# Optimization experiments

Measured on AMD Instinct MI355X. Metric: run time of the kernel, lower is better.

The kernel has to match this reference:

```python
import jax, jax.numpy as jnp
import numpy as np

TEMPERATURE = 0.5


def setup_inputs() -> dict:
    key = jax.random.key(0)
    k1, k2 = jax.random.split(key)
    N, D = 8192, 128
    features = jax.random.normal(k1, (N, D), dtype=jnp.float32)
    labels = jax.random.randint(k2, (N,), 0, 10, dtype=jnp.int64)
    return {"features": features, "labels": labels}


def reference(features, labels):
    # cosine similarity via normalized matmul (fused form of the broadcasted version)
    eps = 1e-8
    norm = jnp.maximum(jnp.linalg.norm(features, axis=-1, keepdims=True), eps)
    fn = features / norm
    sim = jnp.einsum('id,jd->ij', fn, fn) / TEMPERATURE  # [N, N]

    pos_mask = labels[:, None] == labels[None, :]        # [N, N] bool
    pos_f = pos_mask.astype(sim.dtype)
    neg_f = 1.0 - pos_f

    exp_pos = jnp.exp(sim * pos_f)                       # [N, N]
    exp_neg = jnp.sum(jnp.exp(sim * neg_f), axis=1, keepdims=True)  # [N, 1]

    loss_mat = -jnp.log(exp_pos / (exp_pos + exp_neg))   # [N, N]
    # mean over positive entries (jit-safe masked mean)
    num_pos = jnp.sum(pos_f)
    loss = jnp.sum(loss_mat * pos_f) / num_pos
    return loss
```

## Files before the change

### kernel.cpp

```cpp
#include <hip/hip_runtime.h>
#include <hip/hip_bf16.h>
#include <math.h>

#define NROWS 8192
#define DIM 128
#define BM 128
#define BN 128
#define CS 8
#define COLS_PER_SLAB (NROWS / CS)
#define CT_ITERS (COLS_PER_SLAB / BN)
#define RS (NROWS / BM)

typedef __attribute__((ext_vector_type(8))) short bf16x8;
typedef __attribute__((ext_vector_type(4))) float f32x4;

__global__ __launch_bounds__(1024) void k_hist(const int* __restrict__ lab,
                                               int* __restrict__ hist,
                                               float* __restrict__ losssum) {
  __shared__ int sh[16][16];
  const int t = threadIdx.x;
  const int w = t >> 6;
  if ((t & 63) < 16) sh[w][t & 63] = 0;
  __syncthreads();
#pragma unroll
  for (int it = 0; it < NROWS / 1024; ++it)
    atomicAdd(&sh[w][lab[t + it * 1024]], 1);
  __syncthreads();
  if (t < 10) {
    int s = 0;
#pragma unroll
    for (int x = 0; x < 16; ++x) s += sh[x][t];
    hist[t] = s;
  }
  if (t == 10) losssum[0] = 0.f;
}

__global__ __launch_bounds__(256) void k_norm(const float* __restrict__ f,
                                              __hip_bfloat16* __restrict__ fnb) {
  int wave = threadIdx.x >> 6;
  int lane = threadIdx.x & 63;
  int row = blockIdx.x * 4 + wave;
  const float* src = f + (size_t)row * DIM;
  float v0 = src[lane];
  float v1 = src[lane + 64];
  float ss = v0 * v0 + v1 * v1;
#pragma unroll
  for (int o = 32; o > 0; o >>= 1) ss += __shfl_down(ss, o);
  ss = __shfl(ss, 0);
  float inv = 1.0f / fmaxf(sqrtf(ss), 1e-8f);
  __hip_bfloat16* dst = fnb + (size_t)row * DIM;
  dst[lane] = __float2bfloat16(v0 * inv);
  dst[lane + 64] = __float2bfloat16(v1 * inv);
}

__global__ __launch_bounds__(256, 2) void k_main(
    const ushort* __restrict__ fnb, const int* __restrict__ lab,
    float* __restrict__ pneg, float* __restrict__ ppos,
    float* __restrict__ ppos2, float* __restrict__ psim) {
  __shared__ char lds[BM * 256 + BN * 256];
  char* Alds = lds;
  char* Blds = lds + BM * 256;

  const int t = threadIdx.x;
  const int lane = t & 63;
  const int w = t >> 6;
  const int wm = w >> 1;
  const int wn = w & 1;
  const int cs = blockIdx.x;
  const int i0 = blockIdx.y * BM;

  {
    const int4* src = reinterpret_cast<const int4*>(fnb + (size_t)i0 * DIM);
#pragma unroll
    for (int it = 0; it < 8; ++it) {
      int q = t + 256 * it;
      int row = q >> 4, c = q & 15;
      int4 v = src[q];
      *reinterpret_cast<int4*>(Alds + row * 256 + ((c << 4) ^ ((row & 7) << 4))) = v;
    }
  }

  int lr[4][4];
#pragma unroll
  for (int m = 0; m < 4; ++m)
#pragma unroll
    for (int r = 0; r < 4; ++r)
      lr[m][r] = lab[i0 + wm * 64 + m * 16 + (lane >> 4) * 4 + r];

  float a_neg[4][4] = {}, a_pos[4][4] = {}, a_pos2[4][4] = {}, a_sim[4][4] = {};

  for (int ct = 0; ct < CT_ITERS; ++ct) {
    const int j0 = cs * COLS_PER_SLAB + ct * BN;
    __syncthreads();
    {
      const int4* src = reinterpret_cast<const int4*>(fnb + (size_t)j0 * DIM);
#pragma unroll
      for (int it = 0; it < 8; ++it) {
        int q = t + 256 * it;
        int row = q >> 4, c = q & 15;
        int4 v = src[q];
        *reinterpret_cast<int4*>(Blds + row * 256 + ((c << 4) ^ ((row & 7) << 4))) = v;
      }
    }
    __syncthreads();

    f32x4 acc[4][4];
#pragma unroll
    for (int m = 0; m < 4; ++m)
#pragma unroll
      for (int n = 0; n < 4; ++n) acc[m][n] = (f32x4){0.f, 0.f, 0.f, 0.f};

#pragma unroll
    for (int ks = 0; ks < 4; ++ks) {
      const int kb = ks * 64 + ((lane >> 4) << 4);
      bf16x8 af[4], bf[4];
#pragma unroll
      for (int m = 0; m < 4; ++m) {
        int r = wm * 64 + m * 16 + (lane & 15);
        af[m] = *reinterpret_cast<const bf16x8*>(Alds + r * 256 + (kb ^ ((r & 7) << 4)));
      }
#pragma unroll
      for (int n = 0; n < 4; ++n) {
        int r = wn * 64 + n * 16 + (lane & 15);
        bf[n] = *reinterpret_cast<const bf16x8*>(Blds + r * 256 + (kb ^ ((r & 7) << 4)));
      }
#pragma unroll
      for (int m = 0; m < 4; ++m)
#pragma unroll
        for (int n = 0; n < 4; ++n)
          acc[m][n] = __builtin_amdgcn_mfma_f32_16x16x32_bf16(af[m], bf[n], acc[m][n], 0, 0, 0);
    }

#pragma unroll
    for (int n = 0; n < 4; ++n) {
      const int lc = lab[j0 + wn * 64 + n * 16 + (lane & 15)];
#pragma unroll
      for (int m = 0; m < 4; ++m)
#pragma unroll
        for (int r = 0; r < 4; ++r) {
          float s = acc[m][n][r];
          float E = __expf(2.0f * s);
          bool pos = (lr[m][r] == lc);
          a_neg[m][r] += pos ? 0.f : E;
          a_pos[m][r] += pos ? E : 0.f;
          a_pos2[m][r] += pos ? E * E : 0.f;
          a_sim[m][r] += pos ? s : 0.f;
        }
    }
  }

#pragma unroll
  for (int m = 0; m < 4; ++m)
#pragma unroll
    for (int r = 0; r < 4; ++r)
#pragma unroll
      for (int off = 8; off > 0; off >>= 1) {
        a_neg[m][r] += __shfl_xor(a_neg[m][r], off);
        a_pos[m][r] += __shfl_xor(a_pos[m][r], off);
        a_pos2[m][r] += __shfl_xor(a_pos2[m][r], off);
        a_sim[m][r] += __shfl_xor(a_sim[m][r], off);
      }

  __syncthreads();
  float* red = reinterpret_cast<float*>(lds);
  const int g = lane >> 4;
  if (wn == 1 && (lane & 15) == 0) {
#pragma unroll
    for (int m = 0; m < 4; ++m)
#pragma unroll
      for (int r = 0; r < 4; ++r) {
        int rl = wm * 64 + m * 16 + g * 4 + r;
        red[rl * 4 + 0] = a_neg[m][r];
        red[rl * 4 + 1] = a_pos[m][r];
        red[rl * 4 + 2] = a_pos2[m][r];
        red[rl * 4 + 3] = a_sim[m][r];
      }
  }
  __syncthreads();
  if (wn == 0 && (lane & 15) == 0) {
#pragma unroll
    for (int m = 0; m < 4; ++m)
#pragma unroll
      for (int r = 0; r < 4; ++r) {
        int rl = wm * 64 + m * 16 + g * 4 + r;
        int row = i0 + rl;
        pneg[cs * NROWS + row] = a_neg[m][r] + red[rl * 4 + 0];
        ppos[cs * NROWS + row] = a_pos[m][r] + red[rl * 4 + 1];
        ppos2[cs * NROWS + row] = a_pos2[m][r] + red[rl * 4 + 2];
        psim[cs * NROWS + row] = a_sim[m][r] + red[rl * 4 + 3];
      }
  }
}

__global__ __launch_bounds__(1024) void k_rowfinal(
    const float* __restrict__ pneg, const float* __restrict__ ppos,
    const float* __restrict__ ppos2, const float* __restrict__ psim,
    const int* __restrict__ lab, const int* __restrict__ hist,
    float* __restrict__ losssum) {
  __shared__ float sred[1024];
  int i = blockIdx.x * 1024 + threadIdx.x;
  float ns = 0.f, ps = 0.f, ps2 = 0.f, sa = 0.f;
#pragma unroll
  for (int cs = 0; cs < CS; ++cs) {
    ns += pneg[cs * NROWS + i];
    ps += ppos[cs * NROWS + i];
    ps2 += ppos2[cs * NROWS + i];
    sa += psim[cs * NROWS + i];
  }
  float cnt = (float)hist[lab[i]];
  float negtot = ns + cnt;
  float li = cnt * logf(negtot) - 2.f * sa + ps / negtot - ps2 / (2.f * negtot * negtot);
  sred[threadIdx.x] = li;
  __syncthreads();
  for (int s2 = 512; s2 > 0; s2 >>= 1) {
    if (threadIdx.x < s2) sred[threadIdx.x] += sred[threadIdx.x + s2];
    __syncthreads();
  }
  if (threadIdx.x == 0) atomicAdd(losssum, sred[0]);
}

__global__ void k_out(const float* __restrict__ losssum, const int* __restrict__ hist,
                      float* __restrict__ out) {
  if (threadIdx.x == 0) {
    double np = 0.0;
    for (int c = 0; c < 10; ++c) np += (double)hist[c] * (double)hist[c];
    out[0] = (float)((double)losssum[0] / np);
  }
}

extern "C" void kernel_launch(void* const* d_in, const int* in_sizes, int n_in,
                              void* d_out, int out_size, void* d_ws, size_t ws_size,
                              hipStream_t stream) {
  const float* feat = (const float*)d_in[0];
  const int* lab = (const int*)d_in[1];
  float* out = (float*)d_out;

  char* ws = (char*)d_ws;
  __hip_bfloat16* fnb = (__hip_bfloat16*)ws;
  size_t off = (size_t)NROWS * DIM * 2;
  float* pneg = (float*)(ws + off);  off += (size_t)CS * NROWS * 4;
  float* ppos = (float*)(ws + off);  off += (size_t)CS * NROWS * 4;
  float* ppos2 = (float*)(ws + off); off += (size_t)CS * NROWS * 4;
  float* psim = (float*)(ws + off);  off += (size_t)CS * NROWS * 4;
  int* hist = (int*)(ws + off);      off += 64;
  float* losssum = (float*)(ws + off);

  k_hist<<<1, 1024, 0, stream>>>(lab, hist, losssum);
  k_norm<<<NROWS / 4, 256, 0, stream>>>(feat, fnb);
  dim3 grid(CS, RS);
  k_main<<<grid, 256, 0, stream>>>((const ushort*)fnb, lab, pneg, ppos, ppos2, psim);
  k_rowfinal<<<NROWS / 1024, 1024, 0, stream>>>(pneg, ppos, ppos2, psim, lab, hist, losssum);
  k_out<<<1, 64, 0, stream>>>(losssum, hist, out);
}
```

Baseline: 60.53 us.

## Fold temperature scale into normalization and drop squared-positive accumulator

Features are pre-scaled by sqrt(2) during normalization, so the GEMM output is already sim/T and the exp needs no extra multiply. The main kernel now accumulates the total exp sum and derives the negative sum as total minus positive, and it drops the E^2 positive accumulator and its second-order correction term. The histogram kernel is folded into the row-final kernel, which removes one launch, and the cross-wave reduction is simplified. This cuts per-element epilogue ALU work, shuffles and partial-buffer traffic, but it changes the approximation of log(1+x) by dropping a correction term, which may shift accuracy.

```diff
diff --git a/kernel.cpp b/kernel.cpp
--- a/kernel.cpp
+++ b/kernel.cpp
@@ -10,33 +10,15 @@
 #define COLS_PER_SLAB (NROWS / CS)
 #define CT_ITERS (COLS_PER_SLAB / BN)
 #define RS (NROWS / BM)
+#define SQRT2 1.41421356237309515f
 
 typedef __attribute__((ext_vector_type(8))) short bf16x8;
 typedef __attribute__((ext_vector_type(4))) float f32x4;
 
-__global__ __launch_bounds__(1024) void k_hist(const int* __restrict__ lab,
-                                               int* __restrict__ hist,
-                                               float* __restrict__ losssum) {
-  __shared__ int sh[16][16];
-  const int t = threadIdx.x;
-  const int w = t >> 6;
-  if ((t & 63) < 16) sh[w][t & 63] = 0;
-  __syncthreads();
-#pragma unroll
-  for (int it = 0; it < NROWS / 1024; ++it)
-    atomicAdd(&sh[w][lab[t + it * 1024]], 1);
-  __syncthreads();
-  if (t < 10) {
-    int s = 0;
-#pragma unroll
-    for (int x = 0; x < 16; ++x) s += sh[x][t];
-    hist[t] = s;
-  }
-  if (t == 10) losssum[0] = 0.f;
-}
-
 __global__ __launch_bounds__(256) void k_norm(const float* __restrict__ f,
-                                              __hip_bfloat16* __restrict__ fnb) {
+                                              __hip_bfloat16* __restrict__ fnb,
+                                              float* __restrict__ losssum) {
+  if (blockIdx.x == 0 && threadIdx.x == 0) losssum[0] = 0.f;
   int wave = threadIdx.x >> 6;
   int lane = threadIdx.x & 63;
   int row = blockIdx.x * 4 + wave;
@@ -47,7 +29,7 @@
 #pragma unroll
   for (int o = 32; o > 0; o >>= 1) ss += __shfl_down(ss, o);
   ss = __shfl(ss, 0);
-  float inv = 1.0f / fmaxf(sqrtf(ss), 1e-8f);
+  float inv = SQRT2 / fmaxf(sqrtf(ss), 1e-8f);
   __hip_bfloat16* dst = fnb + (size_t)row * DIM;
   dst[lane] = __float2bfloat16(v0 * inv);
   dst[lane + 64] = __float2bfloat16(v1 * inv);
@@ -55,8 +37,7 @@
 
 __global__ __launch_bounds__(256, 2) void k_main(
     const ushort* __restrict__ fnb, const int* __restrict__ lab,
-    float* __restrict__ pneg, float* __restrict__ ppos,
-    float* __restrict__ ppos2, float* __restrict__ psim) {
+    float* __restrict__ ptot, float* __restrict__ ppos, float* __restrict__ psim) {
   __shared__ char lds[BM * 256 + BN * 256];
   char* Alds = lds;
   char* Blds = lds + BM * 256;
@@ -66,6 +47,8 @@
   const int w = t >> 6;
   const int wm = w >> 1;
   const int wn = w & 1;
+  const int g = lane >> 4;
+  const int li16 = lane & 15;
   const int cs = blockIdx.x;
   const int i0 = blockIdx.y * BM;
 
@@ -85,9 +68,9 @@
   for (int m = 0; m < 4; ++m)
 #pragma unroll
     for (int r = 0; r < 4; ++r)
-      lr[m][r] = lab[i0 + wm * 64 + m * 16 + (lane >> 4) * 4 + r];
-
-  float a_neg[4][4] = {}, a_pos[4][4] = {}, a_pos2[4][4] = {}, a_sim[4][4] = {};
+      lr[m][r] = lab[i0 + wm * 64 + m * 16 + g * 4 + r];
+
+  float a_tot[4][4] = {}, a_pos[4][4] = {}, a_sim[4][4] = {};
 
   for (int ct = 0; ct < CT_ITERS; ++ct) {
     const int j0 = cs * COLS_PER_SLAB + ct * BN;
@@ -112,16 +95,16 @@
 
 #pragma unroll
     for (int ks = 0; ks < 4; ++ks) {
-      const int kb = ks * 64 + ((lane >> 4) << 4);
+      const int kb = ks * 64 + (g << 4);
       bf16x8 af[4], bf[4];
 #pragma unroll
       for (int m = 0; m < 4; ++m) {
-        int r = wm * 64 + m * 16 + (lane & 15);
+        int r = wm * 64 + m * 16 + li16;
         af[m] = *reinterpret_cast<const bf16x8*>(Alds + r * 256 + (kb ^ ((r & 7) << 4)));
       }
 #pragma unroll
       for (int n = 0; n < 4; ++n) {
-        int r = wn * 64 + n * 16 + (lane & 15);
+        int r = wn * 64 + n * 16 + li16;
         bf[n] = *reinterpret_cast<const bf16x8*>(Blds + r * 256 + (kb ^ ((r & 7) << 4)));
       }
 #pragma unroll
@@ -133,17 +116,16 @@
 
 #pragma unroll
     for (int n = 0; n < 4; ++n) {
-      const int lc = lab[j0 + wn * 64 + n * 16 + (lane & 15)];
+      const int lc = lab[j0 + wn * 64 + n * 16 + li16];
 #pragma unroll
       for (int m = 0; m < 4; ++m)
 #pragma unroll
         for (int r = 0; r < 4; ++r) {
           float s = acc[m][n][r];
-          float E = __expf(2.0f * s);
+          float E = __expf(s);
           bool pos = (lr[m][r] == lc);
-          a_neg[m][r] += pos ? 0.f : E;
+          a_tot[m][r] += E;
           a_pos[m][r] += pos ? E : 0.f;
-          a_pos2[m][r] += pos ? E * E : 0.f;
           a_sim[m][r] += pos ? s : 0.f;
         }
     }
@@ -155,77 +137,92 @@
     for (int r = 0; r < 4; ++r)
 #pragma unroll
       for (int off = 8; off > 0; off >>= 1) {
-        a_neg[m][r] += __shfl_xor(a_neg[m][r], off);
+        a_tot[m][r] += __shfl_xor(a_tot[m][r], off);
         a_pos[m][r] += __shfl_xor(a_pos[m][r], off);
-        a_pos2[m][r] += __shfl_xor(a_pos2[m][r], off);
         a_sim[m][r] += __shfl_xor(a_sim[m][r], off);
       }
 
   __syncthreads();
-  float* red = reinterpret_cast<float*>(lds);
-  const int g = lane >> 4;
-  if (wn == 1 && (lane & 15) == 0) {
+  float(*red)[2][3] = reinterpret_cast<float(*)[2][3]>(lds);
+  if (li16 == 0) {
 #pragma unroll
     for (int m = 0; m < 4; ++m)
 #pragma unroll
       for (int r = 0; r < 4; ++r) {
         int rl = wm * 64 + m * 16 + g * 4 + r;
-        red[rl * 4 + 0] = a_neg[m][r];
-        red[rl * 4 + 1] = a_pos[m][r];
-        red[rl * 4 + 2] = a_pos2[m][r];
-        red[rl * 4 + 3] = a_sim[m][r];
-      }
-  }
-  __syncthreads();
-  if (wn == 0 && (lane & 15) == 0) {
+        red[rl][wn][0] = a_tot[m][r];
+        red[rl][wn][1] = a_pos[m][r];
+        red[rl][wn][2] = a_sim[m][r];
+      }
+  }
+  __syncthreads();
+  if (wn == 0 && li16 == 0) {
 #pragma unroll
     for (int m = 0; m < 4; ++m)
 #pragma unroll
       for (int r = 0; r < 4; ++r) {
         int rl = wm * 64 + m * 16 + g * 4 + r;
         int row = i0 + rl;
-        pneg[cs * NROWS + row] = a_neg[m][r] + red[rl * 4 + 0];
-        ppos[cs * NROWS + row] = a_pos[m][r] + red[rl * 4 + 1];
-        ppos2[cs * NROWS + row] = a_pos2[m][r] + red[rl * 4 + 2];
-        psim[cs * NROWS + row] = a_sim[m][r] + red[rl * 4 + 3];
+        ptot[(size_t)cs * NROWS + row] = red[rl][0][0] + red[rl][1][0];
+        ppos[(size_t)cs * NROWS + row] = red[rl][0][1] + red[rl][1][1];
+        psim[(size_t)cs * NROWS + row] = red[rl][0][2] + red[rl][1][2];
       }
   }
 }
 
 __global__ __launch_bounds__(1024) void k_rowfinal(
-    const float* __restrict__ pneg, const float* __restrict__ ppos,
-    const float* __restrict__ ppos2, const float* __restrict__ psim,
-    const int* __restrict__ lab, const int* __restrict__ hist,
+    const float* __restrict__ ptot, const float* __restrict__ ppos,
+    const float* __restrict__ psim, const int* __restrict__ lab,
     float* __restrict__ losssum) {
+  __shared__ int sh[16][16];
+  __shared__ int hist_s[16];
   __shared__ float sred[1024];
-  int i = blockIdx.x * 1024 + threadIdx.x;
-  float ns = 0.f, ps = 0.f, ps2 = 0.f, sa = 0.f;
+  const int t = threadIdx.x;
+  const int w = t >> 6;
+  if ((t & 63) < 16) sh[w][t & 63] = 0;
+  __syncthreads();
+#pragma unroll
+  for (int it = 0; it < NROWS / 1024; ++it)
+    atomicAdd(&sh[w][lab[t + it * 1024]], 1);
+  __syncthreads();
+  if (t < 16) {
+    int s = 0;
+#pragma unroll
+    for (int x = 0; x < 16; ++x) s += sh[x][t];
+    hist_s[t] = s;
+  }
+  __syncthreads();
+
+  int i = blockIdx.x * 1024 + t;
+  float st = 0.f, sp = 0.f, sa = 0.f;
 #pragma unroll
   for (int cs = 0; cs < CS; ++cs) {
-    ns += pneg[cs * NROWS + i];
-    ps += ppos[cs * NROWS + i];
-    ps2 += ppos2[cs * NROWS + i];
-    sa += psim[cs * NROWS + i];
-  }
-  float cnt = (float)hist[lab[i]];
-  float negtot = ns + cnt;
-  float li = cnt * logf(negtot) - 2.f * sa + ps / negtot - ps2 / (2.f * negtot * negtot);
-  sred[threadIdx.x] = li;
+    st += ptot[(size_t)cs * NROWS + i];
+    sp += ppos[(size_t)cs * NROWS + i];
+    sa += psim[(size_t)cs * NROWS + i];
+  }
+  float cnt = (float)hist_s[lab[i]];
+  float negtot = st - sp + cnt;
+  float li = cnt * logf(negtot) + sp / negtot - sa;
+  sred[t] = li;
   __syncthreads();
   for (int s2 = 512; s2 > 0; s2 >>= 1) {
-    if (threadIdx.x < s2) sred[threadIdx.x] += sred[threadIdx.x + s2];
+    if (t < s2) sred[t] += sred[t + s2];
     __syncthreads();
   }
-  if (threadIdx.x == 0) atomicAdd(losssum, sred[0]);
-}
-
-__global__ void k_out(const float* __restrict__ losssum, const int* __restrict__ hist,
-                      float* __restrict__ out) {
-  if (threadIdx.x == 0) {
-    double np = 0.0;
-    for (int c = 0; c < 10; ++c) np += (double)hist[c] * (double)hist[c];
-    out[0] = (float)((double)losssum[0] / np);
-  }
+  if (t == 0) {
+    atomicAdd(&losssum[0], sred[0]);
+    if (blockIdx.x == 0) {
+      int np = 0;
+#pragma unroll
+      for (int c = 0; c < 10; ++c) np += hist_s[c] * hist_s[c];
+      losssum[1] = (float)np;
+    }
+  }
+}
+
+__global__ void k_out(const float* __restrict__ losssum, float* __restrict__ out) {
+  if (threadIdx.x == 0) out[0] = losssum[0] / losssum[1];
 }
 
 extern "C" void kernel_launch(void* const* d_in, const int* in_sizes, int n_in,
@@ -238,17 +235,14 @@
   char* ws = (char*)d_ws;
   __hip_bfloat16* fnb = (__hip_bfloat16*)ws;
   size_t off = (size_t)NROWS * DIM * 2;
-  float* pneg = (float*)(ws + off);  off += (size_t)CS * NROWS * 4;
-  float* ppos = (float*)(ws + off);  off += (size_t)CS * NROWS * 4;
-  float* ppos2 = (float*)(ws + off); off += (size_t)CS * NROWS * 4;
-  float* psim = (float*)(ws + off);  off += (size_t)CS * NROWS * 4;
-  int* hist = (int*)(ws + off);      off += 64;
+  float* ptot = (float*)(ws + off); off += (size_t)CS * NROWS * 4;
+  float* ppos = (float*)(ws + off); off += (size_t)CS * NROWS * 4;
+  float* psim = (float*)(ws + off); off += (size_t)CS * NROWS * 4;
   float* losssum = (float*)(ws + off);
 
-  k_hist<<<1, 1024, 0, stream>>>(lab, hist, losssum);
-  k_norm<<<NROWS / 4, 256, 0, stream>>>(feat, fnb);
+  k_norm<<<NROWS / 4, 256, 0, stream>>>(feat, fnb, losssum);
   dim3 grid(CS, RS);
-  k_main<<<grid, 256, 0, stream>>>((const ushort*)fnb, lab, pneg, ppos, ppos2, psim);
-  k_rowfinal<<<NROWS / 1024, 1024, 0, stream>>>(pneg, ppos, ppos2, psim, lab, hist, losssum);
-  k_out<<<1, 64, 0, stream>>>(losssum, hist, out);
-}
+  k_main<<<grid, 256, 0, stream>>>((const ushort*)fnb, lab, ptot, ppos, psim);
+  k_rowfinal<<<NROWS / 1024, 1024, 0, stream>>>(ptot, ppos, psim, lab, losssum);
+  k_out<<<1, 64, 0, stream>>>(losssum, out);
+}
```

Result: faster. 50.93 us (-15.9%).
